# Optimization experiments

Hardware: AMD Instinct MI355X
Metric: run time of the kernel (lower is better)

The kernel has to match this reference:

```python
import jax, jax.numpy as jnp
import numpy as np

DIM = 384
DH = 32
H = DIM // DH          # 12 heads
N_WIN = 3072           # total windows
W_ACT = 1536           # active windows = M
T = 64                 # tokens per window (8x8)
NTOK = W_ACT * T       # 98304 active tokens
N_BLOCK = 9830
MLP = 4 * DIM
EPS = 1e-5


def _layer_norm(h, w, b):
    mu = jnp.mean(h, axis=-1, keepdims=True)
    var = jnp.mean(jnp.square(h - mu), axis=-1, keepdims=True)
    return (h - mu) * jax.lax.rsqrt(var + EPS) * w + b


def setup_inputs() -> dict:
    key = jax.random.key(0)
    ks = jax.random.split(key, 16)
    x = jax.random.normal(ks[0], (N_WIN, T, DIM), jnp.float32)
    # unique active windows, sorted (scatter-restore requires uniqueness)
    index_window = jnp.sort(jax.random.permutation(ks[1], N_WIN)[:W_ACT])
    # full permutation of active tokens into M groups of size S
    index_partition = jax.random.permutation(ks[2], NTOK)
    blocked_index = jax.random.permutation(ks[3], NTOK)[:N_BLOCK]
    s = 0.02
    params = dict(
        ln1_w=jnp.ones((DIM,), jnp.float32), ln1_b=jnp.zeros((DIM,), jnp.float32),
        qkv_w=jax.random.normal(ks[4], (3 * DIM, DIM), jnp.float32) * s,
        qkv_b=jnp.zeros((3 * DIM,), jnp.float32),
        proj_w=jax.random.normal(ks[5], (DIM, DIM), jnp.float32) * s,
        proj_b=jnp.zeros((DIM,), jnp.float32),
        ln2_w=jnp.ones((DIM,), jnp.float32), ln2_b=jnp.zeros((DIM,), jnp.float32),
        fc1_w=jax.random.normal(ks[6], (MLP, DIM), jnp.float32) * s,
        fc1_b=jnp.zeros((MLP,), jnp.float32),
        fc2_w=jax.random.normal(ks[7], (DIM, MLP), jnp.float32) * s,
        fc2_b=jnp.zeros((DIM,), jnp.float32),
    )
    return dict(x=x, index_window=index_window, index_partition=index_partition,
                blocked_index=blocked_index, M=W_ACT, K=jnp.zeros((1,), jnp.int64),
                **params)


def reference(x, index_window, index_partition, blocked_index, M, K,
              ln1_w, ln1_b, qkv_w, qkv_b, proj_w, proj_b,
              ln2_w, ln2_b, fc1_w, fc1_b, fc2_w, fc2_b):
    N, T_, C = x.shape
    scale = DH ** -0.5
    S = index_partition.shape[0] // M

    xn = _layer_norm(x, ln1_w, ln1_b)                      # (N, T, C)
    xw = xn[index_window].reshape(-1, C)                   # (NTOK, C) active tokens
    xp = xw[index_partition].reshape(M, S, C)              # (M, S, C) regrouped
    shortcut = xp

    qkv = (xp @ qkv_w.T + qkv_b).reshape(M, S, H, 3 * DH)  # per-head [q|k|v] chunks
    q, k, v = qkv[..., :DH], qkv[..., DH:2 * DH], qkv[..., 2 * DH:]

    attn = jnp.einsum('mqhd,mkhd->mhqk', q, k) * scale     # (M, H, Sq, Sk)

    # scatter scores into full-size map keyed by KEY token, mask blocked keys, gather back
    amap = jnp.zeros((xw.shape[0], S, H), attn.dtype)      # (NTOK, Sq, H)
    amap = amap.at[index_partition].set(jnp.transpose(attn, (0, 3, 2, 1)).reshape(-1, S, H))
    amap = amap.at[blocked_index].set(-10000.0)
    attn = jnp.transpose(amap[index_partition].reshape(M, S, S, H), (0, 3, 2, 1))
    attn = jax.nn.softmax(attn, axis=-1)

    o = jnp.einsum('mhqk,mkhd->mqhd', attn, v).reshape(M, S, C)
    o = o @ proj_w.T + proj_b

    # sub_layers: [Id, Id(+res), LN, fc1, GELU, fc2(+res)]
    h = shortcut + o
    shortcut = h
    h2 = _layer_norm(h, ln2_w, ln2_b)
    h2 = jax.nn.gelu(h2 @ fc1_w.T + fc1_b, approximate=False)
    h = shortcut + (h2 @ fc2_w.T + fc2_b)

    # scatter-restore: blocked tokens keep their (normed) input values
    XX = xw.at[index_partition].set(h.reshape(-1, C))
    XX = XX.at[blocked_index].set(xw[blocked_index])
    out = xn.at[index_window].set(XX.reshape(M, -1, C))
    return out
```

## Files before the change

kernel.cpp:

```cpp
#include <hip/hip_runtime.h>
#include <hip/hip_bf16.h>

typedef __attribute__((ext_vector_type(8))) short bf16x8;
typedef __attribute__((ext_vector_type(4))) short s16x4;
typedef __attribute__((ext_vector_type(4))) float f32x4;
typedef __attribute__((ext_vector_type(2))) long longx2;

#define NW_   3072
#define WACT_ 1536
#define NTOK_ 98304
#define NBLK_ 9830
#define DIM_  384
#define QKVD_ 1152
#define MLPD_ 1536

__device__ __forceinline__ float bf2f(short s) {
  union { unsigned u; float f; } c;
  c.u = ((unsigned)(unsigned short)s) << 16;
  return c.f;
}
__device__ __forceinline__ short f2bf(float f) {
  union { float f; unsigned u; } c; c.f = f;
  unsigned lsb = (c.u >> 16) & 1u;
  c.u += 0x7fffu + lsb;
  return (short)(c.u >> 16);
}

__device__ __forceinline__ f32x4 mfma8(long a, long b, f32x4 c) {
  return __builtin_amdgcn_mfma_f32_16x16x32_fp8_fp8(a, b, c, 0, 0, 0);
}

__device__ __forceinline__ void gload16(const void* g, void* l) {
  __builtin_amdgcn_global_load_lds(
      (const __attribute__((address_space(1))) unsigned*)g,
      (__attribute__((address_space(3))) unsigned*)l, 16, 0, 0);
}

__device__ __forceinline__ int kperm(int col) {
  int l = (col >> 3) & 7;
  int s = ((l & 3) << 1) | (l >> 2);
  return (col & ~63) + s * 8 + (col & 7);
}

__device__ __forceinline__ void conv8_chunk(const float* __restrict__ src,
                                            unsigned char* __restrict__ dst,
                                            int K, int blk, int tid) {
  int i = (blk * 256 + tid) * 8;
  f32x4 v0 = *(const f32x4*)&src[i];
  f32x4 v1 = *(const f32x4*)&src[i + 4];
  int w0 = __builtin_amdgcn_cvt_pk_fp8_f32(v0[0], v0[1], 0, false);
  w0 = __builtin_amdgcn_cvt_pk_fp8_f32(v0[2], v0[3], w0, true);
  int w1 = __builtin_amdgcn_cvt_pk_fp8_f32(v1[0], v1[1], 0, false);
  w1 = __builtin_amdgcn_cvt_pk_fp8_f32(v1[2], v1[3], w1, true);
  int kro = i % K, row = i / K;
  union { int u[2]; long ll; } p; p.u[0] = w0; p.u[1] = w1;
  *(long*)&dst[(size_t)row * K + kperm(kro)] = p.ll;
}

__global__ __launch_bounds__(256) void pre_k(const float* __restrict__ qkvw,
                                             const float* __restrict__ projw,
                                             const float* __restrict__ fc1w,
                                             const float* __restrict__ fc2w,
                                             unsigned char* __restrict__ qw8,
                                             unsigned char* __restrict__ pw8,
                                             unsigned char* __restrict__ f1w8,
                                             unsigned char* __restrict__ f2w8,
                                             int* win_rank, unsigned* bitmap) {
  const int bid = blockIdx.x, tid = threadIdx.x;
  if (bid < 12) {
    int t = bid * 256 + tid;
    if (t < NW_) { win_rank[t] = -1; bitmap[t] = 0u; }
  } else if (bid < 228) {
    conv8_chunk(qkvw, qw8, 384, bid - 12, tid);
  } else if (bid < 300) {
    conv8_chunk(projw, pw8, 384, bid - 228, tid);
  } else if (bid < 588) {
    conv8_chunk(fc1w, f1w8, 384, bid - 300, tid);
  } else {
    conv8_chunk(fc2w, f2w8, MLPD_, bid - 588, tid);
  }
}

__global__ __launch_bounds__(256) void mapB_k(const int* __restrict__ iw,
                                              const int* __restrict__ blk,
                                              int* win_rank, unsigned* bitmap) {
  int t = blockIdx.x * 256 + threadIdx.x;
  if (t < WACT_) win_rank[iw[t]] = t;
  if (t < NBLK_) { int j = blk[t]; atomicOr(&bitmap[j >> 5], 1u << (j & 31)); }
}

__global__ __launch_bounds__(256) void mapC_k(const int* __restrict__ ip,
                                              const int* __restrict__ iw,
                                              const unsigned* __restrict__ bitmap,
                                              int* inv_ip, int* rowmap) {
  int i = blockIdx.x * 256 + threadIdx.x;
  if (i < NTOK_) {
    int j = ip[i];
    inv_ip[j] = i;
    int blocked = (bitmap[j >> 5] >> (j & 31)) & 1;
    rowmap[i] = blocked ? -1 : (iw[j >> 6] * 64 + (j & 63));
  }
}

__global__ __launch_bounds__(256) void ln1_k(const float* __restrict__ x,
                                             const float* __restrict__ w,
                                             const float* __restrict__ b,
                                             const int* __restrict__ win_rank,
                                             const int* __restrict__ inv_ip,
                                             const unsigned* __restrict__ bitmap,
                                             float* __restrict__ out,
                                             short* __restrict__ xp,
                                             unsigned char* __restrict__ xp8) {
  const int l = threadIdx.x & 31;
  const int tok = blockIdx.x * 8 + (threadIdx.x >> 5);
  const f32x4* xr = (const f32x4*)(x + (size_t)tok * DIM_);
  f32x4 v[3]; float s = 0.f;
#pragma unroll
  for (int j = 0; j < 3; ++j) {
    v[j] = xr[l + 32 * j];
    s += v[j][0] + v[j][1] + v[j][2] + v[j][3];
  }
#pragma unroll
  for (int m = 1; m <= 16; m <<= 1) s += __shfl_xor(s, m, 64);
  float mu = s * (1.0f / DIM_);
  float q = 0.f;
#pragma unroll
  for (int j = 0; j < 3; ++j)
#pragma unroll
    for (int e = 0; e < 4; ++e) { float d = v[j][e] - mu; q += d * d; }
#pragma unroll
  for (int m = 1; m <= 16; m <<= 1) q += __shfl_xor(q, m, 64);
  float rs = rsqrtf(q * (1.0f / DIM_) + 1e-5f);
  f32x4 y[3];
#pragma unroll
  for (int j = 0; j < 3; ++j) {
    f32x4 wv = *(const f32x4*)&w[4 * l + 128 * j];
    f32x4 bv = *(const f32x4*)&b[4 * l + 128 * j];
#pragma unroll
    for (int e = 0; e < 4; ++e) y[j][e] = (v[j][e] - mu) * rs * wv[e] + bv[e];
  }
  int wdw = tok >> 6, t = tok & 63;
  int rank = win_rank[wdw];
  if (rank < 0) {
    f32x4* po = (f32x4*)(out + (size_t)tok * DIM_);
#pragma unroll
    for (int j = 0; j < 3; ++j) po[l + 32 * j] = y[j];
  } else {
    int jdx = (rank << 6) + t;
    int i = inv_ip[jdx];
#pragma unroll
    for (int j = 0; j < 3; ++j) {
      s16x4 o;
#pragma unroll
      for (int e = 0; e < 4; ++e) o[e] = f2bf(y[j][e]);
      *(s16x4*)&xp[(size_t)i * DIM_ + 4 * l + 128 * j] = o;
      int wrd = __builtin_amdgcn_cvt_pk_fp8_f32(y[j][0], y[j][1], 0, false);
      wrd = __builtin_amdgcn_cvt_pk_fp8_f32(y[j][2], y[j][3], wrd, true);
      *(unsigned*)&xp8[(size_t)i * DIM_ + kperm(4 * l + 128 * j)] = (unsigned)wrd;
    }
    if ((bitmap[jdx >> 5] >> (jdx & 31)) & 1) {
      f32x4* po = (f32x4*)(out + (size_t)tok * DIM_);
#pragma unroll
      for (int j = 0; j < 3; ++j) po[l + 32 * j] = y[j];
    }
  }
}

__global__ __launch_bounds__(256) void ln2_k(const short* __restrict__ h,
                                             const float* __restrict__ w,
                                             const float* __restrict__ b,
                                             unsigned char* __restrict__ out8) {
  const int l = threadIdx.x & 31;
  const int tok = blockIdx.x * 8 + (threadIdx.x >> 5);
  const s16x4* xr = (const s16x4*)(h + (size_t)tok * DIM_);
  float v[12]; float s = 0.f;
#pragma unroll
  for (int j = 0; j < 3; ++j) {
    s16x4 rv = xr[l + 32 * j];
#pragma unroll
    for (int e = 0; e < 4; ++e) { v[j * 4 + e] = bf2f(rv[e]); s += v[j * 4 + e]; }
  }
#pragma unroll
  for (int m = 1; m <= 16; m <<= 1) s += __shfl_xor(s, m, 64);
  float mu = s * (1.0f / DIM_);
  float q = 0.f;
#pragma unroll
  for (int e = 0; e < 12; ++e) { float d = v[e] - mu; q += d * d; }
#pragma unroll
  for (int m = 1; m <= 16; m <<= 1) q += __shfl_xor(q, m, 64);
  float rs = rsqrtf(q * (1.0f / DIM_) + 1e-5f);
#pragma unroll
  for (int j = 0; j < 3; ++j) {
    f32x4 wv = *(const f32x4*)&w[4 * l + 128 * j];
    f32x4 bv = *(const f32x4*)&b[4 * l + 128 * j];
    float y[4];
#pragma unroll
    for (int e = 0; e < 4; ++e)
      y[e] = (v[j * 4 + e] - mu) * rs * wv[e] + bv[e];
    int wrd = __builtin_amdgcn_cvt_pk_fp8_f32(y[0], y[1], 0, false);
    wrd = __builtin_amdgcn_cvt_pk_fp8_f32(y[2], y[3], wrd, true);
    int c0 = 4 * l + 128 * j;
    *(unsigned*)&out8[(size_t)tok * DIM_ + kperm(c0)] = (unsigned)wrd;
  }
}

template <int EPI>
__global__ __launch_bounds__(512) void gemmf8_k(const unsigned char* __restrict__ A8,
                                                const unsigned char* __restrict__ B8,
                                                const float* __restrict__ bias,
                                                int K, int nx,
                                                short* __restrict__ Cb,
                                                unsigned char* __restrict__ C8,
                                                const short* __restrict__ add_bf,
                                                const int* __restrict__ rowmap,
                                                float* __restrict__ outf) {
  const int nwg = gridDim.x;
  const int q8 = nwg >> 3;
  const int wg = (blockIdx.x & 7) * q8 + (blockIdx.x >> 3);
  const int ntile = wg % nx, mtile = wg / nx;
  const int tid = threadIdx.x, wid = tid >> 6, lane = tid & 63;
  const int fq = lane >> 4, fr = lane & 15;
  const int wr = wid >> 1, wc = wid & 1;
  __shared__ __align__(16) unsigned char lA[256 * 128];
  __shared__ __align__(16) unsigned char lB[128 * 128];
  const int row0 = mtile * 256, col0 = ntile * 128;
  float bs[4];
#pragma unroll
  for (int nt = 0; nt < 4; ++nt) bs[nt] = bias[col0 + wc * 64 + nt * 16 + fr];
  f32x4 acc[4][4];
#pragma unroll
  for (int a = 0; a < 4; ++a)
#pragma unroll
    for (int c = 0; c < 4; ++c) acc[a][c] = (f32x4){0.f, 0.f, 0.f, 0.f};
  const int nkt = K >> 7;
  for (int kt = 0; kt < nkt; ++kt) {
    const int k0 = kt << 7;
#pragma unroll
    for (int i = 0; i < 4; ++i) {
      int g = i * 512 + tid;
      int r = g >> 3, c8 = g & 7;
      int s8 = c8 ^ (r & 7);
      gload16(A8 + (size_t)(row0 + r) * K + k0 + s8 * 16, (char*)lA + (size_t)g * 16);
    }
#pragma unroll
    for (int i = 0; i < 2; ++i) {
      int g = i * 512 + tid;
      int r = g >> 3, c8 = g & 7;
      int s8 = c8 ^ (r & 7);
      gload16(B8 + (size_t)(col0 + r) * K + k0 + s8 * 16, (char*)lB + (size_t)g * 16);
    }
    __syncthreads();
#pragma unroll
    for (int ss = 0; ss < 2; ++ss) {
      longx2 af[4], bfr[4];
      const int pb = ss * 4 + fq;
#pragma unroll
      for (int mt = 0; mt < 4; ++mt) {
        int r = wr * 64 + mt * 16 + fr;
        int d = pb ^ (r & 7);
        af[mt] = *(const longx2*)&lA[r * 128 + d * 16];
      }
#pragma unroll
      for (int nt = 0; nt < 4; ++nt) {
        int r = wc * 64 + nt * 16 + fr;
        int d = pb ^ (r & 7);
        bfr[nt] = *(const longx2*)&lB[r * 128 + d * 16];
      }
#pragma unroll
      for (int mt = 0; mt < 4; ++mt)
#pragma unroll
        for (int nt = 0; nt < 4; ++nt) {
          acc[mt][nt] = mfma8(af[mt][0], bfr[nt][0], acc[mt][nt]);
          acc[mt][nt] = mfma8(af[mt][1], bfr[nt][1], acc[mt][nt]);
        }
    }
    __syncthreads();
  }
#pragma unroll
  for (int mt = 0; mt < 4; ++mt) {
#pragma unroll
    for (int jj = 0; jj < 4; ++jj) {
      int r = row0 + wr * 64 + mt * 16 + fq * 4 + jj;
      int dmap = 0;
      if (EPI == 3) dmap = rowmap[r];
      if (EPI == 0) {
        float g4[4];
#pragma unroll
        for (int nt = 0; nt < 4; ++nt) g4[nt] = acc[mt][nt][jj] + bs[nt];
        int p01 = __builtin_amdgcn_cvt_pk_fp8_f32(g4[0], g4[1], 0, false);
        int p23 = __builtin_amdgcn_cvt_pk_fp8_f32(g4[2], g4[3], 0, false);
        const size_t rb = (size_t)r * QKVD_ + col0 + wc * 64 + fr;
        C8[rb]      = (unsigned char)(p01 & 0xff);
        C8[rb + 16] = (unsigned char)((p01 >> 8) & 0xff);
        C8[rb + 32] = (unsigned char)(p23 & 0xff);
        C8[rb + 48] = (unsigned char)((p23 >> 8) & 0xff);
      } else if (EPI == 1) {
#pragma unroll
        for (int nt = 0; nt < 4; ++nt) {
          int gcol = col0 + wc * 64 + nt * 16 + fr;
          float v = acc[mt][nt][jj] + bs[nt] + bf2f(add_bf[(size_t)r * DIM_ + gcol]);
          Cb[(size_t)r * DIM_ + gcol] = f2bf(v);
        }
      } else if (EPI == 2) {
        float g4[4];
#pragma unroll
        for (int nt = 0; nt < 4; ++nt) {
          float v = acc[mt][nt][jj] + bs[nt];
          float u = v * (0.79788456f + 0.03567741f * v * v);
          g4[nt] = v * __builtin_amdgcn_rcpf(1.0f + __expf(-2.0f * u));
        }
        int p01 = __builtin_amdgcn_cvt_pk_fp8_f32(g4[0], g4[1], 0, false);
        int p23 = __builtin_amdgcn_cvt_pk_fp8_f32(g4[2], g4[3], 0, false);
        const int C0 = col0 + wc * 64;
        const size_t rb = (size_t)r * MLPD_ + C0 + (fr & 7) + ((fr >> 3) << 4);
        C8[rb]      = (unsigned char)(p01 & 0xff);
        C8[rb + 32] = (unsigned char)((p01 >> 8) & 0xff);
        C8[rb + 8]  = (unsigned char)(p23 & 0xff);
        C8[rb + 40] = (unsigned char)((p23 >> 8) & 0xff);
      } else {
#pragma unroll
        for (int nt = 0; nt < 4; ++nt) {
          int gcol = col0 + wc * 64 + nt * 16 + fr;
          float v = acc[mt][nt][jj] + bs[nt] + bf2f(add_bf[(size_t)r * DIM_ + gcol]);
          if (dmap >= 0) outf[(size_t)dmap * DIM_ + gcol] = v;
        }
      }
    }
  }
}

__global__ __launch_bounds__(256) void attn_k(const unsigned char* __restrict__ qkv8,
                                              const unsigned* __restrict__ bitmap,
                                              const int* __restrict__ ip,
                                              unsigned char* __restrict__ o8) {
  const int flat = (blockIdx.x & 7) * 576 + (blockIdx.x >> 3);
  const int m = flat / 3;
  const int grp = flat % 3;
  const int wid = threadIdx.x >> 6, lane = threadIdx.x & 63;
  const int h = grp * 4 + wid;
  const int fq = lane >> 4, fr = lane & 15;
  __shared__ __align__(16) unsigned char qkvL[24576];
  __shared__ __align__(16) unsigned char Vt[4][32 * 72];
  __shared__ unsigned char flags[64];
  unsigned char (*P)[64 * 72] = (unsigned char (*)[64 * 72])qkvL;

  const unsigned char* rowbase = qkv8 + (size_t)m * 64 * QKVD_ + grp * 384;
#pragma unroll
  for (int i = 0; i < 6; ++i) {
    int g = i * 256 + threadIdx.x;
    int r = g / 24, c16 = g % 24;
    int sc = c16 ^ (r & 7);
    gload16(rowbase + (size_t)r * QKVD_ + sc * 16, (char*)qkvL + (size_t)g * 16);
  }
  if (threadIdx.x < 64) {
    int j = ip[m * 64 + threadIdx.x];
    flags[threadIdx.x] = (unsigned char)((bitmap[j >> 5] >> (j & 31)) & 1);
  }
  __syncthreads();

  const float scale = 0.17677669529663687f;
  int msk[4];
#pragma unroll
  for (int nt = 0; nt < 4; ++nt) msk[nt] = flags[nt * 16 + fr];

  auto ldsc = [&](int r, int c) -> long {
    int slot = (c >> 1) ^ (r & 7);
    return *(const long*)&qkvL[r * 384 + slot * 16 + (c & 1) * 8];
  };

  f32x4 sacc[4][4];
#pragma unroll
  for (int a = 0; a < 4; ++a)
#pragma unroll
    for (int c = 0; c < 4; ++c) sacc[a][c] = (f32x4){0.f, 0.f, 0.f, 0.f};
  long qa[4], kb[4];
#pragma unroll
  for (int mt = 0; mt < 4; ++mt) qa[mt] = ldsc(mt * 16 + fr, wid * 12 + fq);
#pragma unroll
  for (int nt = 0; nt < 4; ++nt) kb[nt] = ldsc(nt * 16 + fr, wid * 12 + 4 + fq);
#pragma unroll
  for (int mt = 0; mt < 4; ++mt)
#pragma unroll
    for (int nt = 0; nt < 4; ++nt)
      sacc[mt][nt] = mfma8(qa[mt], kb[nt], sacc[mt][nt]);
#pragma unroll
  for (int cc = 0; cc < 4; ++cc) {
    long vv = ldsc(lane, wid * 12 + 8 + cc);
    const unsigned char* vb = (const unsigned char*)&vv;
#pragma unroll
    for (int e = 0; e < 8; ++e) Vt[wid][(cc * 8 + e) * 72 + lane] = vb[e];
  }
  __syncthreads();

#pragma unroll
  for (int mt = 0; mt < 4; ++mt)
#pragma unroll
    for (int nt = 0; nt < 4; ++nt) {
      f32x4 sv = sacc[mt][nt];
#pragma unroll
      for (int jj = 0; jj < 4; ++jj)
        sv[jj] = msk[nt] ? -10000.0f : sv[jj] * scale;
      sacc[mt][nt] = sv;
    }
#pragma unroll
  for (int mt = 0; mt < 4; ++mt) {
#pragma unroll
    for (int jj = 0; jj < 4; ++jj) {
      float mx = sacc[mt][0][jj];
#pragma unroll
      for (int nt = 1; nt < 4; ++nt) mx = fmaxf(mx, sacc[mt][nt][jj]);
#pragma unroll
      for (int mm = 1; mm < 16; mm <<= 1) mx = fmaxf(mx, __shfl_xor(mx, mm, 64));
      float sm = 0.f;
      float p[4];
#pragma unroll
      for (int nt = 0; nt < 4; ++nt) {
        p[nt] = __expf(sacc[mt][nt][jj] - mx);
        sm += p[nt];
      }
#pragma unroll
      for (int mm = 1; mm < 16; mm <<= 1) sm += __shfl_xor(sm, mm, 64);
      float inv = 1.0f / sm;
      int rowb = (mt * 16 + fq * 4 + jj) * 72;
      int p01 = __builtin_amdgcn_cvt_pk_fp8_f32(p[0] * inv, p[1] * inv, 0, false);
      int p23 = __builtin_amdgcn_cvt_pk_fp8_f32(p[2] * inv, p[3] * inv, 0, false);
      P[wid][rowb + fr]      = (unsigned char)(p01 & 0xff);
      P[wid][rowb + 16 + fr] = (unsigned char)((p01 >> 8) & 0xff);
      P[wid][rowb + 32 + fr] = (unsigned char)(p23 & 0xff);
      P[wid][rowb + 48 + fr] = (unsigned char)((p23 >> 8) & 0xff);
    }
  }
  f32x4 oacc[4][2];
#pragma unroll
  for (int a = 0; a < 4; ++a)
#pragma unroll
    for (int c = 0; c < 2; ++c) oacc[a][c] = (f32x4){0.f, 0.f, 0.f, 0.f};
#pragma unroll
  for (int ks = 0; ks < 2; ++ks) {
    long pa[4], vb[2];
#pragma unroll
    for (int mt = 0; mt < 4; ++mt)
      pa[mt] = *(const long*)&P[wid][(mt * 16 + fr) * 72 + ks * 32 + fq * 8];
#pragma unroll
    for (int nd = 0; nd < 2; ++nd)
      vb[nd] = *(const long*)&Vt[wid][(nd * 16 + fr) * 72 + ks * 32 + fq * 8];
#pragma unroll
    for (int mt = 0; mt < 4; ++mt)
#pragma unroll
      for (int nd = 0; nd < 2; ++nd)
        oacc[mt][nd] = mfma8(pa[mt], vb[nd], oacc[mt][nd]);
  }
  const int pos0 = kperm(h * 32 + fr);
  const int pos1 = kperm(h * 32 + 16 + fr);
#pragma unroll
  for (int mt = 0; mt < 4; ++mt)
#pragma unroll
    for (int jj = 0; jj < 4; ++jj) {
      int p01 = __builtin_amdgcn_cvt_pk_fp8_f32(oacc[mt][0][jj], oacc[mt][1][jj],
                                                0, false);
      size_t rb = (size_t)(m * 64 + mt * 16 + fq * 4 + jj) * DIM_;
      o8[rb + pos0] = (unsigned char)(p01 & 0xff);
      o8[rb + pos1] = (unsigned char)((p01 >> 8) & 0xff);
    }
}

extern "C" void kernel_launch(void* const* d_in, const int* in_sizes, int n_in,
                              void* d_out, int out_size, void* d_ws, size_t ws_size,
                              hipStream_t stream) {
  const float* x = (const float*)d_in[0];
  const int* iw = (const int*)d_in[1];
  const int* ip = (const int*)d_in[2];
  const int* blk = (const int*)d_in[3];
  const float* ln1w = (const float*)d_in[6];
  const float* ln1b = (const float*)d_in[7];
  const float* qkvw = (const float*)d_in[8];
  const float* qkvb = (const float*)d_in[9];
  const float* projw = (const float*)d_in[10];
  const float* projb = (const float*)d_in[11];
  const float* ln2w = (const float*)d_in[12];
  const float* ln2b = (const float*)d_in[13];
  const float* fc1w = (const float*)d_in[14];
  const float* fc1b = (const float*)d_in[15];
  const float* fc2w = (const float*)d_in[16];
  const float* fc2b = (const float*)d_in[17];
  float* out = (float*)d_out;

  char* ws = (char*)d_ws;
  unsigned char* qkvw8 = (unsigned char*)ws;
  unsigned char* projw8 = (unsigned char*)(ws + 442368);
  unsigned char* fc1w8 = (unsigned char*)(ws + 589824);
  unsigned char* fc2w8 = (unsigned char*)(ws + 1179648);
  int* inv_ip = (int*)(ws + 2211840);
  int* rowmap = inv_ip + NTOK_;
  int* win_rank = rowmap + NTOK_;
  unsigned* bitmap = (unsigned*)(win_rank + NW_);
  short* xp = (short*)(ws + 4349952);
  unsigned char* qkv8 = (unsigned char*)(ws + 79847424);
  unsigned char* t8 = qkv8;
  unsigned char* obuf8 = (unsigned char*)(ws + 306339840);
  unsigned char* ln2buf8 = (unsigned char*)(ws + 344088576);
  unsigned char* xp8 = (unsigned char*)(ws + 381837312);
  short* hbuf = (short*)(ws + 457334784);
  (void)in_sizes; (void)n_in; (void)out_size; (void)ws_size;

  pre_k<<<876, 256, 0, stream>>>(qkvw, projw, fc1w, fc2w, qkvw8, projw8, fc1w8,
                                 fc2w8, win_rank, bitmap);
  mapB_k<<<39, 256, 0, stream>>>(iw, blk, win_rank, bitmap);
  mapC_k<<<NTOK_ / 256, 256, 0, stream>>>(ip, iw, bitmap, inv_ip, rowmap);
  ln1_k<<<(NW_ * 64) / 8, 256, 0, stream>>>(x, ln1w, ln1b, win_rank, inv_ip, bitmap,
                                            out, xp, xp8);
  gemmf8_k<0><<<384 * 9, 512, 0, stream>>>(xp8, qkvw8, qkvb, 384, 9, nullptr,
                                           qkv8, nullptr, nullptr, nullptr);
  attn_k<<<WACT_ * 3, 256, 0, stream>>>(qkv8, bitmap, ip, obuf8);
  gemmf8_k<1><<<384 * 3, 512, 0, stream>>>(obuf8, projw8, projb, 384, 3, hbuf,
                                           nullptr, xp, nullptr, nullptr);
  ln2_k<<<NTOK_ / 8, 256, 0, stream>>>(hbuf, ln2w, ln2b, ln2buf8);
  gemmf8_k<2><<<384 * 12, 512, 0, stream>>>(ln2buf8, fc1w8, fc1b, 384, 12, nullptr,
                                            t8, nullptr, nullptr, nullptr);
  gemmf8_k<3><<<384 * 3, 512, 0, stream>>>(t8, fc2w8, fc2b, MLPD_, 3, nullptr,
                                           nullptr, hbuf, rowmap, out);
}
```

Measured before the change: 609.4 us.

## Fuse projection GEMM with residual add and LayerNorm2 into one kernel

Replaces the proj GEMM (EPI 1) and the separate ln2 kernel with a single kernel in which each workgroup computes a full 64-row by 384-column tile. This lets the residual add and the row-wise LayerNorm statistics be computed in-register with a cross-wave reduction through LDS. The goal is to remove a full read of the bf16 hidden buffer and one kernel launch. In exchange, the fp8 output is written as single bytes, variance uses the E[x^2]-mu^2 form, and the tile shape differs from the tuned 256x128 GEMM, with a larger LDS B tile.

```diff
diff --git a/kernel.cpp b/kernel.cpp
--- a/kernel.cpp
+++ b/kernel.cpp
@@ -166,50 +166,11 @@
   }
 }
 
-__global__ __launch_bounds__(256) void ln2_k(const short* __restrict__ h,
-                                             const float* __restrict__ w,
-                                             const float* __restrict__ b,
-                                             unsigned char* __restrict__ out8) {
-  const int l = threadIdx.x & 31;
-  const int tok = blockIdx.x * 8 + (threadIdx.x >> 5);
-  const s16x4* xr = (const s16x4*)(h + (size_t)tok * DIM_);
-  float v[12]; float s = 0.f;
-#pragma unroll
-  for (int j = 0; j < 3; ++j) {
-    s16x4 rv = xr[l + 32 * j];
-#pragma unroll
-    for (int e = 0; e < 4; ++e) { v[j * 4 + e] = bf2f(rv[e]); s += v[j * 4 + e]; }
-  }
-#pragma unroll
-  for (int m = 1; m <= 16; m <<= 1) s += __shfl_xor(s, m, 64);
-  float mu = s * (1.0f / DIM_);
-  float q = 0.f;
-#pragma unroll
-  for (int e = 0; e < 12; ++e) { float d = v[e] - mu; q += d * d; }
-#pragma unroll
-  for (int m = 1; m <= 16; m <<= 1) q += __shfl_xor(q, m, 64);
-  float rs = rsqrtf(q * (1.0f / DIM_) + 1e-5f);
-#pragma unroll
-  for (int j = 0; j < 3; ++j) {
-    f32x4 wv = *(const f32x4*)&w[4 * l + 128 * j];
-    f32x4 bv = *(const f32x4*)&b[4 * l + 128 * j];
-    float y[4];
-#pragma unroll
-    for (int e = 0; e < 4; ++e)
-      y[e] = (v[j * 4 + e] - mu) * rs * wv[e] + bv[e];
-    int wrd = __builtin_amdgcn_cvt_pk_fp8_f32(y[0], y[1], 0, false);
-    wrd = __builtin_amdgcn_cvt_pk_fp8_f32(y[2], y[3], wrd, true);
-    int c0 = 4 * l + 128 * j;
-    *(unsigned*)&out8[(size_t)tok * DIM_ + kperm(c0)] = (unsigned)wrd;
-  }
-}
-
 template <int EPI>
 __global__ __launch_bounds__(512) void gemmf8_k(const unsigned char* __restrict__ A8,
                                                 const unsigned char* __restrict__ B8,
                                                 const float* __restrict__ bias,
                                                 int K, int nx,
-                                                short* __restrict__ Cb,
                                                 unsigned char* __restrict__ C8,
                                                 const short* __restrict__ add_bf,
                                                 const int* __restrict__ rowmap,
@@ -294,13 +255,6 @@
         C8[rb + 16] = (unsigned char)((p01 >> 8) & 0xff);
         C8[rb + 32] = (unsigned char)(p23 & 0xff);
         C8[rb + 48] = (unsigned char)((p23 >> 8) & 0xff);
-      } else if (EPI == 1) {
-#pragma unroll
-        for (int nt = 0; nt < 4; ++nt) {
-          int gcol = col0 + wc * 64 + nt * 16 + fr;
-          float v = acc[mt][nt][jj] + bs[nt] + bf2f(add_bf[(size_t)r * DIM_ + gcol]);
-          Cb[(size_t)r * DIM_ + gcol] = f2bf(v);
-        }
       } else if (EPI == 2) {
         float g4[4];
 #pragma unroll
@@ -324,6 +278,138 @@
           float v = acc[mt][nt][jj] + bs[nt] + bf2f(add_bf[(size_t)r * DIM_ + gcol]);
           if (dmap >= 0) outf[(size_t)dmap * DIM_ + gcol] = v;
         }
+      }
+    }
+  }
+}
+
+__global__ __launch_bounds__(512, 4) void gemmprojln_k(
+    const unsigned char* __restrict__ A8,
+    const unsigned char* __restrict__ B8,
+    const float* __restrict__ bias,
+    const short* __restrict__ add_bf,
+    const float* __restrict__ lnw,
+    const float* __restrict__ lnb,
+    short* __restrict__ hb,
+    unsigned char* __restrict__ out8) {
+  const int K = 384;
+  const int q8 = gridDim.x >> 3;
+  const int mtile = (blockIdx.x & 7) * q8 + (blockIdx.x >> 3);
+  const int tid = threadIdx.x, wid = tid >> 6, lane = tid & 63;
+  const int fq = lane >> 4, fr = lane & 15;
+  __shared__ __align__(16) unsigned char lA[64 * 128];
+  __shared__ __align__(16) unsigned char lB[384 * 128];
+  __shared__ float red0[8][64], red1[8][64];
+  __shared__ float mu_s[64], rs_s[64];
+  const int row0 = mtile * 64;
+  f32x4 acc[4][3];
+#pragma unroll
+  for (int a = 0; a < 4; ++a)
+#pragma unroll
+    for (int c = 0; c < 3; ++c) acc[a][c] = (f32x4){0.f, 0.f, 0.f, 0.f};
+  for (int kt = 0; kt < 3; ++kt) {
+    const int k0 = kt << 7;
+    {
+      int g = tid;
+      int r = g >> 3, c8 = g & 7;
+      int s8 = c8 ^ (r & 7);
+      gload16(A8 + (size_t)(row0 + r) * K + k0 + s8 * 16, (char*)lA + (size_t)g * 16);
+    }
+#pragma unroll
+    for (int i = 0; i < 6; ++i) {
+      int g = i * 512 + tid;
+      int r = g >> 3, c8 = g & 7;
+      int s8 = c8 ^ (r & 7);
+      gload16(B8 + (size_t)r * K + k0 + s8 * 16, (char*)lB + (size_t)g * 16);
+    }
+    __syncthreads();
+#pragma unroll
+    for (int ss = 0; ss < 2; ++ss) {
+      longx2 af[4], bfr[3];
+      const int pb = ss * 4 + fq;
+#pragma unroll
+      for (int mt = 0; mt < 4; ++mt) {
+        int r = mt * 16 + fr;
+        int d = pb ^ (r & 7);
+        af[mt] = *(const longx2*)&lA[r * 128 + d * 16];
+      }
+#pragma unroll
+      for (int nt = 0; nt < 3; ++nt) {
+        int c = wid * 48 + nt * 16 + fr;
+        int d = pb ^ (c & 7);
+        bfr[nt] = *(const longx2*)&lB[c * 128 + d * 16];
+      }
+#pragma unroll
+      for (int mt = 0; mt < 4; ++mt)
+#pragma unroll
+        for (int nt = 0; nt < 3; ++nt) {
+          acc[mt][nt] = mfma8(af[mt][0], bfr[nt][0], acc[mt][nt]);
+          acc[mt][nt] = mfma8(af[mt][1], bfr[nt][1], acc[mt][nt]);
+        }
+    }
+    __syncthreads();
+  }
+#pragma unroll
+  for (int mt = 0; mt < 4; ++mt) {
+#pragma unroll
+    for (int jj = 0; jj < 4; ++jj) {
+      int rl = mt * 16 + fq * 4 + jj;
+      size_t rg = (size_t)(row0 + rl) * DIM_;
+#pragma unroll
+      for (int nt = 0; nt < 3; ++nt) {
+        int c = wid * 48 + nt * 16 + fr;
+        float v = acc[mt][nt][jj] + bias[c] + bf2f(add_bf[rg + c]);
+        hb[rg + c] = f2bf(v);
+        acc[mt][nt][jj] = v;
+      }
+    }
+  }
+#pragma unroll
+  for (int mt = 0; mt < 4; ++mt) {
+#pragma unroll
+    for (int jj = 0; jj < 4; ++jj) {
+      float s = 0.f, q = 0.f;
+#pragma unroll
+      for (int nt = 0; nt < 3; ++nt) {
+        float v = acc[mt][nt][jj];
+        s += v; q += v * v;
+      }
+#pragma unroll
+      for (int m = 1; m < 16; m <<= 1) {
+        s += __shfl_xor(s, m, 64);
+        q += __shfl_xor(q, m, 64);
+      }
+      if (fr == 0) {
+        int rl = mt * 16 + fq * 4 + jj;
+        red0[wid][rl] = s;
+        red1[wid][rl] = q;
+      }
+    }
+  }
+  __syncthreads();
+  if (tid < 64) {
+    float S = 0.f, Q = 0.f;
+#pragma unroll
+    for (int w = 0; w < 8; ++w) { S += red0[w][tid]; Q += red1[w][tid]; }
+    float mu = S * (1.0f / DIM_);
+    float var = Q * (1.0f / DIM_) - mu * mu;
+    mu_s[tid] = mu;
+    rs_s[tid] = rsqrtf(var + 1e-5f);
+  }
+  __syncthreads();
+#pragma unroll
+  for (int mt = 0; mt < 4; ++mt) {
+#pragma unroll
+    for (int jj = 0; jj < 4; ++jj) {
+      int rl = mt * 16 + fq * 4 + jj;
+      size_t rg = (size_t)(row0 + rl) * DIM_;
+      float mu = mu_s[rl], rs = rs_s[rl];
+#pragma unroll
+      for (int nt = 0; nt < 3; ++nt) {
+        int c = wid * 48 + nt * 16 + fr;
+        float y = (acc[mt][nt][jj] - mu) * rs * lnw[c] + lnb[c];
+        int pk = __builtin_amdgcn_cvt_pk_fp8_f32(y, y, 0, false);
+        out8[rg + kperm(c)] = (unsigned char)(pk & 0xff);
       }
     }
   }
@@ -509,14 +595,13 @@
   mapC_k<<<NTOK_ / 256, 256, 0, stream>>>(ip, iw, bitmap, inv_ip, rowmap);
   ln1_k<<<(NW_ * 64) / 8, 256, 0, stream>>>(x, ln1w, ln1b, win_rank, inv_ip, bitmap,
                                             out, xp, xp8);
-  gemmf8_k<0><<<384 * 9, 512, 0, stream>>>(xp8, qkvw8, qkvb, 384, 9, nullptr,
+  gemmf8_k<0><<<384 * 9, 512, 0, stream>>>(xp8, qkvw8, qkvb, 384, 9,
                                            qkv8, nullptr, nullptr, nullptr);
   attn_k<<<WACT_ * 3, 256, 0, stream>>>(qkv8, bitmap, ip, obuf8);
-  gemmf8_k<1><<<384 * 3, 512, 0, stream>>>(obuf8, projw8, projb, 384, 3, hbuf,
-                                           nullptr, xp, nullptr, nullptr);
-  ln2_k<<<NTOK_ / 8, 256, 0, stream>>>(hbuf, ln2w, ln2b, ln2buf8);
-  gemmf8_k<2><<<384 * 12, 512, 0, stream>>>(ln2buf8, fc1w8, fc1b, 384, 12, nullptr,
+  gemmprojln_k<<<1536, 512, 0, stream>>>(obuf8, projw8, projb, xp, ln2w, ln2b,
+                                         hbuf, ln2buf8);
+  gemmf8_k<2><<<384 * 12, 512, 0, stream>>>(ln2buf8, fc1w8, fc1b, 384, 12,
                                             t8, nullptr, nullptr, nullptr);
-  gemmf8_k<3><<<384 * 3, 512, 0, stream>>>(t8, fc2w8, fc2b, MLPD_, 3, nullptr,
+  gemmf8_k<3><<<384 * 3, 512, 0, stream>>>(t8, fc2w8, fc2b, MLPD_, 3,
                                            nullptr, hbuf, rowmap, out);
 }
```

Result: no change. 614.5 us (+0.8%).
